# Optimization experiments

Measured on AMD Instinct MI355X. Metric: run time of the kernel, lower is better.

The kernel has to match this reference:

```python
import jax, jax.numpy as jnp
import numpy as np

N_NODES = 50000
N_EDGES = 800000
NODE_DIM = 128
HIDDEN = 256
LATENT = 128
COND = 5


def setup_inputs() -> dict:
    key = jax.random.key(0)
    ks = jax.random.split(key, 10)
    s = lambda d: 1.0 / np.sqrt(d)
    return {
        "node_features": jax.random.normal(ks[0], (N_NODES, NODE_DIM), jnp.float32),
        "conditions": jax.random.normal(ks[1], (COND,), jnp.float32),
        "src": jax.random.randint(ks[2], (N_EDGES,), 0, N_NODES, jnp.int32),
        "dst": jax.random.randint(ks[3], (N_EDGES,), 0, N_NODES, jnp.int32),
        "W1": jax.random.normal(ks[4], (NODE_DIM, HIDDEN), jnp.float32) * s(NODE_DIM),
        "b1": jnp.zeros((HIDDEN,), jnp.float32),
        "W2": jax.random.normal(ks[5], (HIDDEN, HIDDEN), jnp.float32) * s(HIDDEN),
        "b2": jnp.zeros((HIDDEN,), jnp.float32),
        "Wfc": jax.random.normal(ks[6], (HIDDEN + COND, LATENT), jnp.float32) * s(HIDDEN + COND),
        "bfc": jnp.zeros((LATENT,), jnp.float32),
        "Wmean": jax.random.normal(ks[7], (LATENT, LATENT), jnp.float32) * s(LATENT),
        "bmean": jnp.zeros((LATENT,), jnp.float32),
        "Wlogvar": jax.random.normal(ks[8], (LATENT, LATENT), jnp.float32) * s(LATENT),
        "blogvar": jnp.zeros((LATENT,), jnp.float32),
    }


def _graph_conv(x, src, dst, W, b, n_nodes):
    # gather source-node features along edges, sum-aggregate onto targets,
    # then linear transform: standard GraphConv (sum aggregation)
    agg = jax.ops.segment_sum(x[src], dst, num_segments=n_nodes)  # [N, d]
    return agg @ W + b


def reference(node_features, conditions, src, dst,
              W1, b1, W2, b2, Wfc, bfc, Wmean, bmean, Wlogvar, blogvar):
    n = node_features.shape[0]
    x = jax.nn.relu(_graph_conv(node_features, src, dst, W1, b1, n))  # [N, H]
    x = jax.nn.relu(_graph_conv(x, src, dst, W2, b2, n))              # [N, H]
    pooled = jnp.mean(x, axis=0)                                      # [H]
    h = jax.nn.relu(jnp.concatenate([pooled, conditions], axis=-1) @ Wfc + bfc)
    z_mean = h @ Wmean + bmean
    z_logvar = h @ Wlogvar + blogvar
    return z_mean, z_logvar
```

## Files before the change

### kernel.cpp

```cpp
#include <hip/hip_runtime.h>

#define N_NODES   50000
#define N_EDGES   800000
#define NODE_DIM  128
#define HIDDEN    256
#define LATENT    128
#define COND      5

#define NB        196
#define P1_CHUNK  4096
#define P1_GRID   ((N_EDGES + P1_CHUNK - 1) / P1_CHUNK)

typedef unsigned int uint;
typedef unsigned short ushort;
typedef unsigned char uchar;

typedef __attribute__((ext_vector_type(8))) short bf16x8;
typedef __attribute__((ext_vector_type(4))) float f32x4;

static __device__ __forceinline__ ushort f32_to_bf16(float f) {
    union { float f; uint u; } v; v.f = f;
    uint r = v.u + 0x7FFF + ((v.u >> 16) & 1);
    return (ushort)(r >> 16);
}
static __device__ __forceinline__ uint pack_bf16(float lo, float hi) {
    return (uint)f32_to_bf16(lo) | ((uint)f32_to_bf16(hi) << 16);
}

static __device__ __forceinline__ void gload_lds16(const void* g, void* l) {
    __builtin_amdgcn_global_load_lds(
        (const __attribute__((address_space(1))) unsigned int*)(unsigned long long)(uintptr_t)g,
        (__attribute__((address_space(3))) unsigned int*)(unsigned int)(uintptr_t)l,
        16, 0, 0);
}


#if __has_builtin(__builtin_amdgcn_cvt_pk_f32_fp8) && __has_builtin(__builtin_amdgcn_cvt_pk_fp8_f32)
#define HW_FP8 1
#endif

#ifndef HW_FP8
static __device__ __forceinline__ float dec1_fp8(uint b) {
    uint sgn = b & 0x80, mag = b & 0x7f;
    float v;
    if (mag >= 8) {
        union { uint u; float f; } t;
        t.u = (((mag >> 3) + 120) << 23) | ((mag & 7) << 20);
        v = t.f;
    } else {
        v = (float)mag * 0.001953125f;
    }
    return sgn ? -v : v;
}
static __device__ __forceinline__ uchar enc1_fp8(float f) {
    float a = fabsf(f);
    uint s = (f < 0.f) ? 0x80u : 0u;
    if (!(a >= 0.015625f)) {
        int q = (int)(a * 512.f + 0.5f);
        if (q > 7) q = 7;
        return (uchar)(s | (uint)q);
    }
    if (a >= 448.f) return (uchar)(s | 0x7E);
    union { float f; uint u; } t; t.f = a;
    uint e = (t.u >> 23) - 120;
    uint m = (t.u >> 20) & 7;
    uint rem = t.u & 0xFFFFF;
    uint v = (e << 3) | m;
    if (rem > 0x80000 || (rem == 0x80000 && (v & 1))) v++;
    if (v > 0x7E) v = 0x7E;
    return (uchar)(s | v);
}
#endif

static __device__ __forceinline__ void dec4_add(uint u, float* acc) {
#ifdef HW_FP8
    auto lo = __builtin_amdgcn_cvt_pk_f32_fp8((int)u, false);
    auto hi = __builtin_amdgcn_cvt_pk_f32_fp8((int)u, true);
    acc[0] += lo[0]; acc[1] += lo[1]; acc[2] += hi[0]; acc[3] += hi[1];
#else
    acc[0] += dec1_fp8(u & 0xff);
    acc[1] += dec1_fp8((u >> 8) & 0xff);
    acc[2] += dec1_fp8((u >> 16) & 0xff);
    acc[3] += dec1_fp8(u >> 24);
#endif
}
static __device__ __forceinline__ void dec2_add(uint u, float* acc) {
#ifdef HW_FP8
    auto lo = __builtin_amdgcn_cvt_pk_f32_fp8((int)u, false);
    acc[0] += lo[0]; acc[1] += lo[1];
#else
    acc[0] += dec1_fp8(u & 0xff);
    acc[1] += dec1_fp8((u >> 8) & 0xff);
#endif
}
static __device__ __forceinline__ uint enc2_fp8(float a, float b) {
#ifdef HW_FP8
    return (uint)__builtin_amdgcn_cvt_pk_fp8_f32(a, b, 0, false) & 0xFFFFu;
#else
    return (uint)enc1_fp8(a) | ((uint)enc1_fp8(b) << 8);
#endif
}
static __device__ __forceinline__ uchar enc1(float v) {
#ifdef HW_FP8
    return (uchar)(__builtin_amdgcn_cvt_pk_fp8_f32(v, v, 0, false) & 0xff);
#else
    return enc1_fp8(v);
#endif
}


#define NF4   (N_NODES * NODE_DIM / 4)
#define PREP1 (NF4 + NODE_DIM * HIDDEN)
#define PREP2 (PREP1 + HIDDEN * HIDDEN)
#define PREP3 (PREP2 + HIDDEN)
#define PREP4 (PREP3 + NB)
#define PREP5 (PREP4 + NB)

__global__ void prep_kernel(const float* __restrict__ nf,
                            const float* __restrict__ W1, const float* __restrict__ W2,
                            uchar* __restrict__ nf_fp8,
                            ushort* __restrict__ Wst1, ushort* __restrict__ Wst2,
                            float* __restrict__ pooled,
                            int* __restrict__ bcount, int* __restrict__ bcursor2) {
    int id = blockIdx.x * blockDim.x + threadIdx.x;
    if (id < NF4) {
        float4 v = reinterpret_cast<const float4*>(nf)[id];
        uint w = enc2_fp8(v.x, v.y) | (enc2_fp8(v.z, v.w) << 16);
        reinterpret_cast<uint*>(nf_fp8)[id] = w;
    } else if (id < PREP1) {
        int i = id - NF4;
        int k = i >> 8, c = i & 255;
        int idx = ((((k >> 5) * 16) + (((k & 31) >> 3) * 4 + (c >> 6))) * 64 + (c & 63)) * 8 + (k & 7);
        Wst1[idx] = f32_to_bf16(W1[i]);
    } else if (id < PREP2) {
        int i = id - PREP1;
        int k = i >> 8, c = i & 255;
        int idx = ((((k >> 5) * 16) + (((k & 31) >> 3) * 4 + (c >> 6))) * 64 + (c & 63)) * 8 + (k & 7);
        Wst2[idx] = f32_to_bf16(W2[i]);
    } else if (id < PREP3) {
        pooled[id - PREP2] = 0.f;
    } else if (id < PREP4) {
        bcount[id - PREP3] = 0;
    } else if (id < PREP5) {
        bcursor2[id - PREP4] = 0;
    }
}


__global__ __launch_bounds__(256) void bcount_kernel(const int* __restrict__ dst,
                                                     int* __restrict__ bcount) {
    __shared__ int cnt[NB];
    const int t = threadIdx.x;
    for (int i = t; i < NB; i += 256) cnt[i] = 0;
    __syncthreads();
    const int base = blockIdx.x * P1_CHUNK;
#pragma unroll
    for (int i = 0; i < 16; ++i) {
        int e = base + i * 256 + t;
        if (e < N_EDGES) atomicAdd(&cnt[dst[e] >> 8], 1);
    }
    __syncthreads();
    for (int i = t; i < NB; i += 256)
        if (cnt[i] > 0) atomicAdd(&bcount[i], cnt[i]);
}

__global__ __launch_bounds__(256) void bwrite_kernel(const int* __restrict__ src,
                                                     const int* __restrict__ dst,
                                                     const int* __restrict__ bcount,
                                                     int* __restrict__ bcursor2,
                                                     uint* __restrict__ pair_buf) {
    __shared__ int s[256];
    __shared__ int cnt[NB];
    __shared__ int gbase[NB];
    const int t = threadIdx.x;
    s[t] = (t < NB) ? bcount[t] : 0;
    __syncthreads();
    for (int off = 1; off < 256; off <<= 1) {
        int v = (t >= off) ? s[t - off] : 0;
        __syncthreads();
        s[t] += v;
        __syncthreads();
    }
    for (int i = t; i < NB; i += 256) cnt[i] = 0;
    __syncthreads();

    const int base = blockIdx.x * P1_CHUNK;
    uint pk[16];
    int  bk[16], lr[16];
    bool ok[16];
#pragma unroll
    for (int i = 0; i < 16; ++i) {
        int e = base + i * 256 + t;
        ok[i] = e < N_EDGES;
        if (ok[i]) {
            int sv = src[e], d = dst[e];
            pk[i] = (uint)sv | ((uint)d << 16);
            bk[i] = d >> 8;
        }
    }
#pragma unroll
    for (int i = 0; i < 16; ++i)
        if (ok[i]) lr[i] = atomicAdd(&cnt[bk[i]], 1);
    __syncthreads();
    if (t < NB) {
        int c = cnt[t];
        if (c > 0) gbase[t] = ((t > 0) ? s[t - 1] : 0) + atomicAdd(&bcursor2[t], c);
    }
    __syncthreads();
#pragma unroll
    for (int i = 0; i < 16; ++i)
        if (ok[i]) pair_buf[gbase[bk[i]] + lr[i]] = pk[i];
}

__global__ __launch_bounds__(256) void csrloc_kernel(const uint* __restrict__ pair_buf,
                                                     const int* __restrict__ bcount,
                                                     int* __restrict__ offsets,
                                                     ushort* __restrict__ csr) {
    __shared__ int s[256];
    __shared__ int lcnt[256];
    __shared__ int loff[256];
    __shared__ int lcur[256];
    const int t = threadIdx.x;
    const int b = blockIdx.x;
    s[t] = (t < NB) ? bcount[t] : 0;
    __syncthreads();
    for (int off = 1; off < 256; off <<= 1) {
        int v = (t >= off) ? s[t - off] : 0;
        __syncthreads();
        s[t] += v;
        __syncthreads();
    }
    const int e0 = (b > 0) ? s[b - 1] : 0;
    const int e1 = s[b];
    lcnt[t] = 0;
    lcur[t] = 0;
    __syncthreads();

    for (int j = e0 + t; j < e1; j += 256)
        atomicAdd(&lcnt[(pair_buf[j] >> 16) & 255], 1);
    __syncthreads();

    const int myc = lcnt[t];
    s[t] = myc;
    __syncthreads();
    for (int off = 1; off < 256; off <<= 1) {
        int v = (t >= off) ? s[t - off] : 0;
        __syncthreads();
        s[t] += v;
        __syncthreads();
    }
    const int lofft = s[t] - myc;
    loff[t] = lofft;
    const int node = (b << 8) + t;
    if (node < N_NODES) offsets[node] = e0 + lofft;
    if (b == 0 && t == 0) offsets[N_NODES] = N_EDGES;
    __syncthreads();

    for (int j = e0 + t; j < e1; j += 256) {
        uint p = pair_buf[j];
        int dl = (int)(p >> 16) & 255;
        int r = atomicAdd(&lcur[dl], 1);
        csr[e0 + loff[dl] + r] = (ushort)(p & 0xFFFFu);
    }
}


template <int D>
__global__ __launch_bounds__(256) void agg_kernel(const uchar* __restrict__ x,
                                                  const int* __restrict__ offsets,
                                                  const ushort* __restrict__ csr,
                                                  ushort* __restrict__ out) {
    constexpr int BPL = D / 64;
    int node = (blockIdx.x * blockDim.x + threadIdx.x) >> 6;
    int lane = threadIdx.x & 63;
    if (node >= N_NODES) return;
    int j0 = __builtin_amdgcn_readfirstlane(offsets[node]);
    int j1 = __builtin_amdgcn_readfirstlane(offsets[node + 1]);

    float acc[BPL];
#pragma unroll
    for (int i = 0; i < BPL; ++i) acc[i] = 0.f;

    const uchar* base = x + lane * BPL;
    const int il = lane & 15;

    int idxv = (j0 + il < j1) ? (int)csr[j0 + il] : 0;

    for (int jb = j0; jb < j1; jb += 16) {
        int idxn = (jb + 16 + il < j1) ? (int)csr[jb + 16 + il] : 0;
        int n = j1 - jb; n = (n > 16) ? 16 : n;
        uint u[16];
        if (n == 16) {
#pragma unroll
            for (int i = 0; i < 16; ++i) {
                int s = __shfl(idxv, i);
                if constexpr (BPL == 4)
                    u[i] = *reinterpret_cast<const uint*>(base + (size_t)s * D);
                else
                    u[i] = *reinterpret_cast<const ushort*>(base + (size_t)s * D);
            }
#pragma unroll
            for (int i = 0; i < 16; ++i) {
                if constexpr (BPL == 4) dec4_add(u[i], acc); else dec2_add(u[i], acc);
            }
        } else {
#pragma unroll
            for (int i = 0; i < 16; ++i) {
                if (i < n) {
                    int s = __shfl(idxv, i);
                    if constexpr (BPL == 4)
                        u[i] = *reinterpret_cast<const uint*>(base + (size_t)s * D);
                    else
                        u[i] = *reinterpret_cast<const ushort*>(base + (size_t)s * D);
                }
            }
#pragma unroll
            for (int i = 0; i < 16; ++i) {
                if (i < n) {
                    if constexpr (BPL == 4) dec4_add(u[i], acc); else dec2_add(u[i], acc);
                }
            }
        }
        idxv = idxn;
    }

    if constexpr (BPL == 4) {
        uint2 o;
        o.x = pack_bf16(acc[0], acc[1]);
        o.y = pack_bf16(acc[2], acc[3]);
        *reinterpret_cast<uint2*>(out + (size_t)node * D + lane * 4) = o;
    } else {
        *reinterpret_cast<uint*>(out + (size_t)node * D + lane * 2) = pack_bf16(acc[0], acc[1]);
    }
}


template <int K, bool POOL>
__global__ __launch_bounds__(256) void gemm_lds_kernel(const ushort* __restrict__ A,
                                                       const ushort* __restrict__ Wst,
                                                       const float* __restrict__ bias,
                                                       uchar* __restrict__ Xout,
                                                       float* __restrict__ pooled) {
    constexpr int BUFB  = 18432;
    constexpr int NSTEP = K / 32;
    __shared__ uchar lds_raw[2 * BUFB];

    const int t    = threadIdx.x;
    const int lane = t & 63;
    const int wv   = t >> 6;
    const int row0 = blockIdx.x * 32;
    const int fr   = lane & 15;
    const int kgl  = lane >> 4;

    auto stage = [&](int buf, int ks) {
#pragma unroll
        for (int j = 0; j < 5; ++j) {
            const int c = wv * 5 + j;
            if (c < 2) {
                gload_lds16(A + (size_t)(row0 + c * 16 + (lane >> 2)) * K + ks * 32 + (lane & 3) * 8,
                            &lds_raw[buf * BUFB + c * 1024]);
            } else if (c < 18) {
                const int w = c - 2;
                gload_lds16(Wst + ((size_t)ks * 16 + w) * 512 + lane * 8,
                            &lds_raw[buf * BUFB + 2048 + w * 1024]);
            }
        }
    };

    f32x4 acc[2][4];
#pragma unroll
    for (int rt = 0; rt < 2; ++rt)
#pragma unroll
        for (int ct = 0; ct < 4; ++ct)
            acc[rt][ct] = (f32x4){0.f, 0.f, 0.f, 0.f};

    stage(0, 0);
#pragma unroll
    for (int ks = 0; ks < NSTEP; ++ks) {
        const int buf = ks & 1;
        if (ks + 1 < NSTEP) stage(buf ^ 1, ks + 1);
        __syncthreads();
        const uchar* bb = &lds_raw[buf * BUFB];
        bf16x8 af[2], bfv[4];
#pragma unroll
        for (int rt = 0; rt < 2; ++rt)
            af[rt] = *reinterpret_cast<const bf16x8*>(bb + rt * 1024 + fr * 64 + kgl * 16);
#pragma unroll
        for (int ct = 0; ct < 4; ++ct)
            bfv[ct] = *reinterpret_cast<const bf16x8*>(bb + 2048 + (kgl * 4 + wv) * 1024 + (ct * 16 + fr) * 16);
#pragma unroll
        for (int rt = 0; rt < 2; ++rt)
#pragma unroll
            for (int ct = 0; ct < 4; ++ct)
                acc[rt][ct] = __builtin_amdgcn_mfma_f32_16x16x32_bf16(af[rt], bfv[ct], acc[rt][ct], 0, 0, 0);
        __syncthreads();
    }

    const int col0 = wv * 64;
    float bcol[4];
#pragma unroll
    for (int ct = 0; ct < 4; ++ct) bcol[ct] = bias[col0 + ct * 16 + fr];
    const int mrow = (lane >> 4) * 4;

    if constexpr (POOL) {
        float cs[4] = {0.f, 0.f, 0.f, 0.f};
#pragma unroll
        for (int rt = 0; rt < 2; ++rt) {
#pragma unroll
            for (int e = 0; e < 4; ++e) {
                int m = row0 + rt * 16 + mrow + e;
                if (m < N_NODES) {
#pragma unroll
                    for (int ct = 0; ct < 4; ++ct)
                        cs[ct] += fmaxf(acc[rt][ct][e] + bcol[ct], 0.f);
                }
            }
        }
#pragma unroll
        for (int ct = 0; ct < 4; ++ct) {
            cs[ct] += __shfl_xor(cs[ct], 16);
            cs[ct] += __shfl_xor(cs[ct], 32);
        }
        if (lane < 16) {
#pragma unroll
            for (int ct = 0; ct < 4; ++ct)
                atomicAdd(&pooled[col0 + ct * 16 + lane], cs[ct]);
        }
    } else {
#pragma unroll
        for (int rt = 0; rt < 2; ++rt) {
#pragma unroll
            for (int e = 0; e < 4; ++e) {
                int m = row0 + rt * 16 + mrow + e;
                if (m < N_NODES) {
#pragma unroll
                    for (int ct = 0; ct < 4; ++ct) {
                        float v = fmaxf(acc[rt][ct][e] + bcol[ct], 0.f);
                        Xout[(size_t)m * HIDDEN + col0 + ct * 16 + fr] = enc1(v);
                    }
                }
            }
        }
    }
}


__global__ void head_kernel(const float* __restrict__ pooled_sum, const float* __restrict__ cond,
                            const float* __restrict__ Wfc, const float* __restrict__ bfc,
                            const float* __restrict__ Wmean, const float* __restrict__ bmean,
                            const float* __restrict__ Wlogvar, const float* __restrict__ blogvar,
                            float* __restrict__ out) {
    __shared__ float v[HIDDEN + COND];
    __shared__ float h[LATENT];
    int t = threadIdx.x;
    if (t < HIDDEN) v[t] = pooled_sum[t] * (1.0f / N_NODES);
    if (t < COND) v[HIDDEN + t] = cond[t];
    __syncthreads();
    if (t < LATENT) {
        float s = bfc[t];
        for (int k = 0; k < HIDDEN + COND; ++k) s += v[k] * Wfc[k * LATENT + t];
        h[t] = fmaxf(s, 0.f);
    }
    __syncthreads();
    if (t < LATENT) {
        float s = bmean[t];
        for (int k = 0; k < LATENT; ++k) s += h[k] * Wmean[k * LATENT + t];
        out[t] = s;
    } else {
        int j = t - LATENT;
        float s = blogvar[j];
        for (int k = 0; k < LATENT; ++k) s += h[k] * Wlogvar[k * LATENT + j];
        out[LATENT + j] = s;
    }
}


extern "C" void kernel_launch(void* const* d_in, const int* in_sizes, int n_in,
                              void* d_out, int out_size, void* d_ws, size_t ws_size,
                              hipStream_t stream) {
    const float* node_features = (const float*)d_in[0];
    const float* conditions    = (const float*)d_in[1];
    const int*   src           = (const int*)d_in[2];
    const int*   dst           = (const int*)d_in[3];
    const float* W1  = (const float*)d_in[4];
    const float* b1  = (const float*)d_in[5];
    const float* W2  = (const float*)d_in[6];
    const float* b2  = (const float*)d_in[7];
    const float* Wfc = (const float*)d_in[8];
    const float* bfc = (const float*)d_in[9];
    const float* Wmean   = (const float*)d_in[10];
    const float* bmean   = (const float*)d_in[11];
    const float* Wlogvar = (const float*)d_in[12];
    const float* blogvar = (const float*)d_in[13];
    float* out = (float*)d_out;

    size_t o = 0;
    auto alloc = [&](size_t bytes) {
        void* p = (char*)d_ws + o;
        o += (bytes + 255) & ~(size_t)255;
        return p;
    };
    int* offsets   = (int*)alloc((size_t)(N_NODES + 1) * 4);
    int* bcount    = (int*)alloc((size_t)NB * 4);
    int* bcursor2  = (int*)alloc((size_t)NB * 4);
    uint* pair_buf = (uint*)alloc((size_t)N_EDGES * 4);
    ushort* csr    = (ushort*)alloc((size_t)N_EDGES * 2);
    float* pooled  = (float*)alloc(HIDDEN * 4);
    ushort* Wst1   = (ushort*)alloc((size_t)HIDDEN * NODE_DIM * 2);
    ushort* Wst2   = (ushort*)alloc((size_t)HIDDEN * HIDDEN * 2);
    uchar* nf_fp8  = (uchar*)alloc((size_t)N_NODES * NODE_DIM);
    uchar* x1_fp8  = (uchar*)alloc((size_t)N_NODES * HIDDEN);
    ushort* agg1   = (ushort*)alloc((size_t)(N_NODES + 64) * NODE_DIM * 2);
    ushort* agg2   = (ushort*)alloc((size_t)(N_NODES + 64) * HIDDEN * 2);

    prep_kernel<<<(PREP5 + 255) / 256, 256, 0, stream>>>(
        node_features, W1, W2, nf_fp8, Wst1, Wst2, pooled, bcount, bcursor2);

    bcount_kernel<<<P1_GRID, 256, 0, stream>>>(dst, bcount);
    bwrite_kernel<<<P1_GRID, 256, 0, stream>>>(src, dst, bcount, bcursor2, pair_buf);
    csrloc_kernel<<<NB, 256, 0, stream>>>(pair_buf, bcount, offsets, csr);

    const int AGG_GRID  = (N_NODES * 64 + 255) / 256;
    const int GEMM_GRID = (N_NODES + 31) / 32;

    agg_kernel<NODE_DIM><<<AGG_GRID, 256, 0, stream>>>(nf_fp8, offsets, csr, agg1);
    gemm_lds_kernel<NODE_DIM, false><<<GEMM_GRID, 256, 0, stream>>>(agg1, Wst1, b1, x1_fp8, nullptr);

    agg_kernel<HIDDEN><<<AGG_GRID, 256, 0, stream>>>(x1_fp8, offsets, csr, agg2);
    gemm_lds_kernel<HIDDEN, true><<<GEMM_GRID, 256, 0, stream>>>(agg2, Wst2, b2, nullptr, pooled);

    head_kernel<<<1, 256, 0, stream>>>(pooled, conditions, Wfc, bfc,
                                       Wmean, bmean, Wlogvar, blogvar, out);
}
```

Before: 175.1 us.

## Make GEMMs persistent with LDS-resident weight half and swizzled A tiles

The two dense GEMM kernels become persistent: each block loads half of the weight matrix (one column half) into LDS once, then loops over 64-row tiles of the aggregated features with double-buffered A staging. A reads use an XOR swizzle to cut LDS bank conflicts, and the pooled column sums build up across tiles so each block issues its atomics only once. The goal is to stop restaging weights for every 32-row tile and to shrink the launched grid. In exchange, LDS use per block is much larger (up to about 128KB for K=256), which limits occupancy.

New measurement: 142.6 us. -18.6%, faster.

```diff
diff --git a/kernel.cpp b/kernel.cpp
--- a/kernel.cpp
+++ b/kernel.cpp
@@ -336,86 +336,124 @@
 
 
 template <int K, bool POOL>
-__global__ __launch_bounds__(256) void gemm_lds_kernel(const ushort* __restrict__ A,
+__global__ __launch_bounds__(256) void gemm_res_kernel(const ushort* __restrict__ A,
                                                        const ushort* __restrict__ Wst,
                                                        const float* __restrict__ bias,
                                                        uchar* __restrict__ Xout,
-                                                       float* __restrict__ pooled) {
-    constexpr int BUFB  = 18432;
+                                                       float* __restrict__ pooled,
+                                                       int nblk) {
     constexpr int NSTEP = K / 32;
-    __shared__ uchar lds_raw[2 * BUFB];
+    constexpr int WB    = NSTEP * 8 * 1024;
+    constexpr int AB    = NSTEP * 4 * 1024;
+    constexpr int NT    = (N_NODES + 63) / 64;
+    __shared__ uchar lds[WB + 2 * AB];
 
     const int t    = threadIdx.x;
     const int lane = t & 63;
     const int wv   = t >> 6;
-    const int row0 = blockIdx.x * 32;
     const int fr   = lane & 15;
     const int kgl  = lane >> 4;
-
-    auto stage = [&](int buf, int ks) {
-#pragma unroll
-        for (int j = 0; j < 5; ++j) {
-            const int c = wv * 5 + j;
-            if (c < 2) {
-                gload_lds16(A + (size_t)(row0 + c * 16 + (lane >> 2)) * K + ks * 32 + (lane & 3) * 8,
-                            &lds_raw[buf * BUFB + c * 1024]);
-            } else if (c < 18) {
-                const int w = c - 2;
-                gload_lds16(Wst + ((size_t)ks * 16 + w) * 512 + lane * 8,
-                            &lds_raw[buf * BUFB + 2048 + w * 1024]);
-            }
+    const int colhalf = blockIdx.x & 1;
+    const int stride  = nblk >> 1;
+
+    const int kx = (lane & 3) ^ ((lane >> 3) & 3);
+
+#pragma unroll
+    for (int j = 0; j < NSTEP * 2; ++j) {
+        const int lc = wv * (NSTEP * 2) + j;
+        const int ks = lc >> 3, r = lc & 7;
+        const int kg = r >> 1, ccl = r & 1;
+        gload_lds16(Wst + ((size_t)ks * 16 + kg * 4 + colhalf * 2 + ccl) * 512 + lane * 8,
+                    &lds[lc * 1024]);
+    }
+
+    auto stageA = [&](int buf, int row0) {
+#pragma unroll
+        for (int j = 0; j < NSTEP; ++j) {
+            const int c  = wv * NSTEP + j;
+            const int ks = c >> 2, rt = c & 3;
+            gload_lds16(A + (size_t)(row0 + rt * 16 + (lane >> 2)) * K + ks * 32 + kx * 8,
+                        &lds[WB + buf * AB + c * 1024]);
         }
     };
 
-    f32x4 acc[2][4];
-#pragma unroll
-    for (int rt = 0; rt < 2; ++rt)
-#pragma unroll
-        for (int ct = 0; ct < 4; ++ct)
-            acc[rt][ct] = (f32x4){0.f, 0.f, 0.f, 0.f};
-
-    stage(0, 0);
-#pragma unroll
-    for (int ks = 0; ks < NSTEP; ++ks) {
-        const int buf = ks & 1;
-        if (ks + 1 < NSTEP) stage(buf ^ 1, ks + 1);
-        __syncthreads();
-        const uchar* bb = &lds_raw[buf * BUFB];
-        bf16x8 af[2], bfv[4];
+    const int rowsel = (wv & 1) * 2;
+    const int colsel = wv >> 1;
+    const int col0   = colhalf * 128 + colsel * 64;
+    float bcol[4];
+#pragma unroll
+    for (int ct = 0; ct < 4; ++ct) bcol[ct] = bias[col0 + ct * 16 + fr];
+    const int mrow = kgl * 4;
+    const int aswz = (kgl ^ ((fr >> 1) & 3)) * 16;
+
+    float cs[4] = {0.f, 0.f, 0.f, 0.f};
+
+    int tile = blockIdx.x >> 1;
+    stageA(0, tile * 64);
+    __syncthreads();
+
+    for (int buf = 0; tile < NT; tile += stride, buf ^= 1) {
+        const int tn = tile + stride;
+        if (tn < NT) stageA(buf ^ 1, tn * 64);
+
+        f32x4 acc[2][4];
 #pragma unroll
         for (int rt = 0; rt < 2; ++rt)
-            af[rt] = *reinterpret_cast<const bf16x8*>(bb + rt * 1024 + fr * 64 + kgl * 16);
-#pragma unroll
-        for (int ct = 0; ct < 4; ++ct)
-            bfv[ct] = *reinterpret_cast<const bf16x8*>(bb + 2048 + (kgl * 4 + wv) * 1024 + (ct * 16 + fr) * 16);
-#pragma unroll
-        for (int rt = 0; rt < 2; ++rt)
 #pragma unroll
             for (int ct = 0; ct < 4; ++ct)
-                acc[rt][ct] = __builtin_amdgcn_mfma_f32_16x16x32_bf16(af[rt], bfv[ct], acc[rt][ct], 0, 0, 0);
-        __syncthreads();
-    }
-
-    const int col0 = wv * 64;
-    float bcol[4];
-#pragma unroll
-    for (int ct = 0; ct < 4; ++ct) bcol[ct] = bias[col0 + ct * 16 + fr];
-    const int mrow = (lane >> 4) * 4;
-
-    if constexpr (POOL) {
-        float cs[4] = {0.f, 0.f, 0.f, 0.f};
-#pragma unroll
-        for (int rt = 0; rt < 2; ++rt) {
-#pragma unroll
-            for (int e = 0; e < 4; ++e) {
-                int m = row0 + rt * 16 + mrow + e;
-                if (m < N_NODES) {
-#pragma unroll
-                    for (int ct = 0; ct < 4; ++ct)
-                        cs[ct] += fmaxf(acc[rt][ct][e] + bcol[ct], 0.f);
+                acc[rt][ct] = (f32x4){0.f, 0.f, 0.f, 0.f};
+
+        const uchar* ab = &lds[WB + buf * AB];
+#pragma unroll
+        for (int ks = 0; ks < NSTEP; ++ks) {
+            bf16x8 af[2], bfv[4];
+#pragma unroll
+            for (int rt = 0; rt < 2; ++rt)
+                af[rt] = *reinterpret_cast<const bf16x8*>(ab + (ks * 4 + rowsel + rt) * 1024 + fr * 64 + aswz);
+#pragma unroll
+            for (int ct = 0; ct < 4; ++ct)
+                bfv[ct] = *reinterpret_cast<const bf16x8*>(&lds[(ks * 8 + kgl * 2 + colsel) * 1024 + (ct * 16 + fr) * 16]);
+#pragma unroll
+            for (int rt = 0; rt < 2; ++rt)
+#pragma unroll
+                for (int ct = 0; ct < 4; ++ct)
+                    acc[rt][ct] = __builtin_amdgcn_mfma_f32_16x16x32_bf16(af[rt], bfv[ct], acc[rt][ct], 0, 0, 0);
+        }
+
+        const int rowbase = tile * 64 + (wv & 1) * 32;
+        if constexpr (POOL) {
+#pragma unroll
+            for (int rt = 0; rt < 2; ++rt) {
+#pragma unroll
+                for (int e = 0; e < 4; ++e) {
+                    int m = rowbase + rt * 16 + mrow + e;
+                    if (m < N_NODES) {
+#pragma unroll
+                        for (int ct = 0; ct < 4; ++ct)
+                            cs[ct] += fmaxf(acc[rt][ct][e] + bcol[ct], 0.f);
+                    }
                 }
             }
-        }
+        } else {
+#pragma unroll
+            for (int rt = 0; rt < 2; ++rt) {
+#pragma unroll
+                for (int e = 0; e < 4; ++e) {
+                    int m = rowbase + rt * 16 + mrow + e;
+                    if (m < N_NODES) {
+#pragma unroll
+                        for (int ct = 0; ct < 4; ++ct) {
+                            float v = fmaxf(acc[rt][ct][e] + bcol[ct], 0.f);
+                            Xout[(size_t)m * HIDDEN + col0 + ct * 16 + fr] = enc1(v);
+                        }
+                    }
+                }
+            }
+        }
+        __syncthreads();
+    }
+
+    if constexpr (POOL) {
 #pragma unroll
         for (int ct = 0; ct < 4; ++ct) {
             cs[ct] += __shfl_xor(cs[ct], 16);
@@ -425,21 +463,6 @@
 #pragma unroll
             for (int ct = 0; ct < 4; ++ct)
                 atomicAdd(&pooled[col0 + ct * 16 + lane], cs[ct]);
-        }
-    } else {
-#pragma unroll
-        for (int rt = 0; rt < 2; ++rt) {
-#pragma unroll
-            for (int e = 0; e < 4; ++e) {
-                int m = row0 + rt * 16 + mrow + e;
-                if (m < N_NODES) {
-#pragma unroll
-                    for (int ct = 0; ct < 4; ++ct) {
-                        float v = fmaxf(acc[rt][ct][e] + bcol[ct], 0.f);
-                        Xout[(size_t)m * HIDDEN + col0 + ct * 16 + fr] = enc1(v);
-                    }
-                }
-            }
         }
     }
 }
@@ -520,14 +543,15 @@
     bwrite_kernel<<<P1_GRID, 256, 0, stream>>>(src, dst, bcount, bcursor2, pair_buf);
     csrloc_kernel<<<NB, 256, 0, stream>>>(pair_buf, bcount, offsets, csr);
 
-    const int AGG_GRID  = (N_NODES * 64 + 255) / 256;
-    const int GEMM_GRID = (N_NODES + 31) / 32;
+    const int AGG_GRID = (N_NODES * 64 + 255) / 256;
+    const int G1_BLK = 512;
+    const int G2_BLK = 256;
 
     agg_kernel<NODE_DIM><<<AGG_GRID, 256, 0, stream>>>(nf_fp8, offsets, csr, agg1);
-    gemm_lds_kernel<NODE_DIM, false><<<GEMM_GRID, 256, 0, stream>>>(agg1, Wst1, b1, x1_fp8, nullptr);
+    gemm_res_kernel<NODE_DIM, false><<<G1_BLK, 256, 0, stream>>>(agg1, Wst1, b1, x1_fp8, nullptr, G1_BLK);
 
     agg_kernel<HIDDEN><<<AGG_GRID, 256, 0, stream>>>(x1_fp8, offsets, csr, agg2);
-    gemm_lds_kernel<HIDDEN, true><<<GEMM_GRID, 256, 0, stream>>>(agg2, Wst2, b2, nullptr, pooled);
+    gemm_res_kernel<HIDDEN, true><<<G2_BLK, 256, 0, stream>>>(agg2, Wst2, b2, nullptr, pooled, G2_BLK);
 
     head_kernel<<<1, 256, 0, stream>>>(pooled, conditions, Wfc, bfc,
                                        Wmean, bmean, Wlogvar, blogvar, out);
```
